# Optimization experiments

Measured on AMD Instinct MI355X. Metric: run time of the kernel, lower is better.

The kernel has to match this reference:

```python
import jax, jax.numpy as jnp
import numpy as np

# yolov5 non_max_suppression defaults (from forward's input_parameters.get defaults)
CONF_THRES = 0.25
IOU_THRES = 0.45
MAX_DET = 1000        # max detections returned per image
TOP_K = 4096          # fixed candidate count entering greedy NMS (jit-friendly stand-in for max_nms)
MAX_WH = 7680.0       # per-class box offset so NMS is class-aware (yolov5 trick)


def setup_inputs() -> dict:
    key = jax.random.key(0)
    k1, k2, k3, k4 = jax.random.split(key, 4)
    B, N, NC = 16, 25200, 80  # 640x640 yolov5 -> 25200 anchors, 80 COCO classes
    xy = jax.random.uniform(k1, (B, N, 2)) * 640.0            # box centers in pixels
    wh = jax.random.uniform(k2, (B, N, 2)) * 160.0 + 4.0       # box sizes
    obj = jax.random.uniform(k3, (B, N, 1))                    # objectness
    cls = jax.random.uniform(k4, (B, N, NC))                   # class scores
    pred = jnp.concatenate([xy, wh, obj, cls], axis=-1)        # [B, N, 85]
    return {"pred": pred}


def _xywh2xyxy(x):
    xy, wh = x[..., :2], x[..., 2:4]
    return jnp.concatenate([xy - wh * 0.5, xy + wh * 0.5], axis=-1)


def _iou_one_vs_all(box, boxes):
    # box [4], boxes [K,4], xyxy
    lt = jnp.maximum(box[:2], boxes[:, :2])
    rb = jnp.minimum(box[2:], boxes[:, 2:])
    wh = jnp.clip(rb - lt, 0.0)
    inter = wh[:, 0] * wh[:, 1]
    a1 = (box[2] - box[0]) * (box[3] - box[1])
    a2 = (boxes[:, 2] - boxes[:, 0]) * (boxes[:, 3] - boxes[:, 1])
    return inter / (a1 + a2 - inter + 1e-7)


def _nms_single(pred):
    # pred [N, 5+nc] raw yolov5 output for one image
    obj = pred[:, 4:5]
    scores_all = pred[:, 5:] * obj                 # conf = obj_conf * cls_conf
    conf = scores_all.max(axis=-1)                 # best-class confidence [N]
    cls = scores_all.argmax(axis=-1).astype(pred.dtype)
    boxes = _xywh2xyxy(pred[:, :4])                # [N,4] xyxy

    valid = conf > CONF_THRES
    s = jnp.where(valid, conf, -1.0)
    order = jnp.argsort(-s)[:TOP_K]                # top candidates by score
    b = boxes[order]                               # [K,4]
    sc = s[order]                                  # [K]
    c = cls[order]                                 # [K]
    ob = b + c[:, None] * MAX_WH                   # class-offset boxes for class-aware NMS

    ar = jnp.arange(TOP_K)

    def step(supp, i):
        alive = (~supp[i]) & (sc[i] > 0.0)
        iou = _iou_one_vs_all(ob[i], ob)
        supp = supp | (alive & (iou > IOU_THRES) & (ar > i))
        return supp, alive

    _, keep = jax.lax.scan(step, jnp.zeros(TOP_K, dtype=bool), ar)

    fs = jnp.where(keep, sc, -1.0)
    idx = jnp.argsort(-fs)[:MAX_DET]               # kept boxes, score-sorted
    det = jnp.concatenate([b[idx], fs[idx][:, None], c[idx][:, None]], axis=-1)  # [max_det,6]
    ok = fs[idx] > 0.0
    return jnp.where(ok[:, None], det, 0.0)        # zero-padded [max_det, 6] (x1,y1,x2,y2,conf,cls)


def reference(pred):
    # [B, max_det, 6] padded detections per image
    return jax.vmap(_nms_single)(pred)
```

## Files before the change

### kernel.cpp

```cpp
#include <hip/hip_runtime.h>

#define BATCH  16
#define NPRED  25200
#define NCLS   80
#define CDIM   85
#define TOPK   4096
#define NBUCK  4096
#define MAXDET 1000
#define CONF_T 0.25f
#define IOU_T  0.45f
#define MAXWH  7680.0f
#define ORD_BASE 0xBE800000u

typedef unsigned long long u64;
typedef unsigned int u32;
typedef unsigned short u16;
typedef unsigned char u8;

__device__ __forceinline__ u64 umax64(u64 a, u64 b) { return a > b ? a : b; }
__device__ __forceinline__ u64 umin64(u64 a, u64 b) { return a < b ? a : b; }

__device__ __forceinline__ void cx_u64(u64* a, int i, int p, bool desc) {
    u64 x = a[i], y = a[p];
    if (desc ? (x < y) : (x > y)) { a[i] = y; a[p] = x; }
}


__device__ void hybrid_sort4096_desc(u64 r[4], u64* a) {
    const int tid = threadIdx.x;
    for (int k = 2; k <= 4096; k <<= 1) {
        if (k >= 512) {
            int jmax = (k >> 1) > 2048 ? 2048 : (k >> 1);
#pragma unroll
            for (int e = 0; e < 4; ++e) a[4 * tid + e] = r[e];
            __syncthreads();
            for (int j = jmax; j >= 256; j >>= 1) {
#pragma unroll
                for (int t2 = 0; t2 < 2; ++t2) {
                    int q = (t2 << 10) | tid;
                    int i = ((q & ~(j - 1)) << 1) | (q & (j - 1));
                    cx_u64(a, i, i | j, (i & k) == 0);
                }
                __syncthreads();
            }
#pragma unroll
            for (int e = 0; e < 4; ++e) r[e] = a[4 * tid + e];
            __syncthreads();
        }
        {
            int jstart = (k >> 1) > 128 ? 128 : (k >> 1);
            bool desc = (((4 * tid) & k) == 0);
            for (int j = jstart; j >= 4; j >>= 1) {
                int m = j >> 2;
                bool take_max = (((tid & m) == 0) == desc);
#pragma unroll
                for (int e = 0; e < 4; ++e) {
                    u64 v = __shfl_xor(r[e], m, 64);
                    r[e] = take_max ? umax64(r[e], v) : umin64(r[e], v);
                }
            }
        }
        if (k >= 4) {
            bool desc = (((4 * tid) & k) == 0);
            u64 x0 = r[0], x2 = r[2];
            r[0] = desc ? umax64(x0, x2) : umin64(x0, x2);
            r[2] = desc ? umin64(x0, x2) : umax64(x0, x2);
            u64 x1 = r[1], x3 = r[3];
            r[1] = desc ? umax64(x1, x3) : umin64(x1, x3);
            r[3] = desc ? umin64(x1, x3) : umax64(x1, x3);
        }
        {
            bool d01 = (((4 * tid + 0) & k) == 0);
            bool d23 = (((4 * tid + 2) & k) == 0);
            u64 x0 = r[0], x1 = r[1];
            r[0] = d01 ? umax64(x0, x1) : umin64(x0, x1);
            r[1] = d01 ? umin64(x0, x1) : umax64(x0, x1);
            u64 x2 = r[2], x3 = r[3];
            r[2] = d23 ? umax64(x2, x3) : umin64(x2, x3);
            r[3] = d23 ? umin64(x2, x3) : umax64(x2, x3);
        }
    }
}

__device__ void wave_sort256_desc(u64 r[4]) {
    const int lane = threadIdx.x & 63;
    for (int k = 2; k <= 256; k <<= 1) {
        int jstart = (k >> 1) > 128 ? 128 : (k >> 1);
        bool desc = (((4 * lane) & k) == 0);
        for (int j = jstart; j >= 4; j >>= 1) {
            int m = j >> 2;
            bool take_max = (((lane & m) == 0) == desc);
#pragma unroll
            for (int e = 0; e < 4; ++e) {
                u64 v = __shfl_xor(r[e], m, 64);
                r[e] = take_max ? umax64(r[e], v) : umin64(r[e], v);
            }
        }
        if (k >= 4) {
            u64 x0 = r[0], x2 = r[2];
            r[0] = desc ? umax64(x0, x2) : umin64(x0, x2);
            r[2] = desc ? umin64(x0, x2) : umax64(x0, x2);
            u64 x1 = r[1], x3 = r[3];
            r[1] = desc ? umax64(x1, x3) : umin64(x1, x3);
            r[3] = desc ? umin64(x1, x3) : umax64(x1, x3);
        }
        {
            bool d01 = (((4 * lane + 0) & k) == 0);
            bool d23 = (((4 * lane + 2) & k) == 0);
            u64 x0 = r[0], x1 = r[1];
            r[0] = d01 ? umax64(x0, x1) : umin64(x0, x1);
            r[1] = d01 ? umin64(x0, x1) : umax64(x0, x1);
            u64 x2 = r[2], x3 = r[3];
            r[2] = d23 ? umax64(x2, x3) : umin64(x2, x3);
            r[3] = d23 ? umin64(x2, x3) : umax64(x2, x3);
        }
    }
}


__global__ __launch_bounds__(256) void k1_score(const float* __restrict__ pred,
                                                u64* __restrict__ keys,
                                                u32* __restrict__ ghist) {
    const int lane = threadIdx.x & 63;
    const int l16 = lane & 15;
    const long long gw = (long long)blockIdx.x * 4 + (threadIdx.x >> 6);
    const long long rowIdx = gw * 4 + (lane >> 4);
    const int b = (int)(rowIdx / NPRED);
    const int n = (int)(rowIdx - (long long)b * NPRED);
    const float* row = pred + rowIdx * CDIM;
    float obj = row[4];
    u64 m = 0ull;
#pragma unroll
    for (int k = 0; k < 5; ++k) {
        int c = l16 + 16 * k;
        float v = row[5 + c] * obj;
        u64 mk = ((u64)(__float_as_uint(v) | 0x80000000u) << 32) | (u64)(u32)(NCLS - 1 - c);
        if (mk > m) m = mk;
    }
#pragma unroll
    for (int o = 8; o > 0; o >>= 1) {
        u64 other = __shfl_xor(m, o, 64);
        if (other > m) m = other;
    }
    if (l16 == 0) {
        float best = __uint_as_float((u32)(m >> 32) & 0x7FFFFFFFu);
        int cls = (NCLS - 1) - (int)(m & 0x7Fu);
        float s = (best > CONF_T) ? best : -1.0f;
        u32 u = __float_as_uint(s);
        u32 ord = (u & 0x80000000u) ? ~u : (u | 0x80000000u);
        keys[rowIdx] = ((u64)ord << 32) | ((u64)(u32)(32767 - n) << 7) | (u64)(u32)cls;
        if (ord > ORD_BASE)
            atomicAdd(&ghist[b * NBUCK + ((ord - ORD_BASE - 1u) >> 12)], 1u);
    }
}


__global__ __launch_bounds__(1024) void k2cs(const u64* __restrict__ keys,
                                             const u32* __restrict__ ghist,
                                             u64* __restrict__ topSorted) {
    __shared__ u64 smem[4096];
    __shared__ u64 side[1024];
    __shared__ u32 wsum[16];
    __shared__ int sh_T, sh_C1, sh_R, c1pos, sidepos;
    const int b = blockIdx.x;
    const int tid = threadIdx.x;
    const int lane = tid & 63;
    const int wid = tid >> 6;

    u32 h[4];
    u32 tsum = 0;
#pragma unroll
    for (int e = 0; e < 4; ++e) {
        h[e] = ghist[b * NBUCK + (NBUCK - 1 - (4 * tid + e))];
        tsum += h[e];
    }
    u32 inc = tsum;
    for (int o = 1; o < 64; o <<= 1) {
        u32 v = __shfl_up(inc, o, 64);
        if (lane >= o) inc += v;
    }
    if (lane == 63) wsum[wid] = inc;
    __syncthreads();
    if (tid == 0) {
        u32 run = 0;
        for (int i = 0; i < 16; ++i) { u32 t = wsum[i]; wsum[i] = run; run += t; }
        sh_T = -1; sh_C1 = (int)run; sh_R = 0;
        c1pos = 0; sidepos = 0;
    }
    __syncthreads();
    {
        u32 cum = wsum[wid] + (inc - tsum);
#pragma unroll
        for (int e = 0; e < 4; ++e) {
            if (h[e] > 0 && cum < (u32)TOPK && cum + h[e] >= (u32)TOPK) {
                sh_T = NBUCK - 1 - (4 * tid + e);
                sh_C1 = (int)cum;
                sh_R = TOPK - (int)cum;
            }
            cum += h[e];
        }
    }
    __syncthreads();
    const int T = sh_T, C1 = sh_C1, R = sh_R;

    for (int i = tid; i < 4096; i += 1024) smem[i] = 0ull;
    side[tid] = 0ull;
    __syncthreads();
    const u64* kb = keys + (long long)b * NPRED;
    for (int n = tid; n < NPRED; n += 1024) {
        u64 key = kb[n];
        u32 hi = (u32)(key >> 32);
        if (hi > ORD_BASE) {
            int bt = (int)((hi - ORD_BASE - 1u) >> 12);
            if (bt > T) {
                int slot = atomicAdd(&c1pos, 1);
                smem[slot] = key;
            } else if (bt == T) {
                int s2 = atomicAdd(&sidepos, 1);
                if (s2 < 1024) side[s2] = key;
            }
        }
    }
    __syncthreads();

    if (R > 0) {
        int cntT = sidepos;
        if (cntT <= 256) {
            if (wid == 0) {
                u64 r[4];
#pragma unroll
                for (int e = 0; e < 4; ++e) r[e] = side[4 * lane + e];
                wave_sort256_desc(r);
#pragma unroll
                for (int e = 0; e < 4; ++e) side[4 * lane + e] = r[e];
            }
        } else {
            for (int k = 2; k <= 1024; k <<= 1) {
                for (int j = k >> 1; j >= 1; j >>= 1) {
                    if (tid < 512) {
                        int q = tid;
                        int i = ((q & ~(j - 1)) << 1) | (q & (j - 1));
                        cx_u64(side, i, i | j, (i & k) == 0);
                    }
                    __syncthreads();
                }
            }
        }
        __syncthreads();
        if (tid < R) smem[C1 + tid] = side[tid];
    }
    __syncthreads();

    u64 r[4];
#pragma unroll
    for (int e = 0; e < 4; ++e) r[e] = smem[4 * tid + e];
    hybrid_sort4096_desc(r, smem);
#pragma unroll
    for (int e = 0; e < 4; ++e) topSorted[(long long)b * TOPK + 4 * tid + e] = r[e];
}


__global__ __launch_bounds__(256) void k3a_build(const float* __restrict__ pred,
                                                 const u64* __restrict__ topSorted,
                                                 float4* __restrict__ ob,
                                                 u8* __restrict__ clsb,
                                                 u32* __restrict__ count) {
    const int idx = blockIdx.x * 256 + threadIdx.x;
    const int b = idx >> 12;
    u64 key = topSorted[idx];
    u32 hi = (u32)(key >> 32);
    u8 c = 0xFF;
    if (hi > 0x80000000u) {
        int n = 32767 - (int)((key >> 7) & 0x7FFFu);
        int ci = (int)(key & 0x7Fu);
        const float* row = pred + ((long long)b * NPRED + n) * CDIM;
        float x = row[0], y = row[1], w = row[2], h = row[3];
        float off = (float)ci * MAXWH;
        float4 o;
        o.x = (x - w * 0.5f) + off;
        o.y = (y - h * 0.5f) + off;
        o.z = (x + w * 0.5f) + off;
        o.w = (y + h * 0.5f) + off;
        ob[idx] = o;
        c = (u8)ci;
        atomicAdd(&count[b * NCLS + ci], 1u);
    }
    clsb[idx] = c;
}


__global__ __launch_bounds__(64) void k3g_gather(const u8* __restrict__ clsb,
                                                 const u32* __restrict__ count,
                                                 u32* __restrict__ startg,
                                                 u16* __restrict__ segIdx) {
    const int b = blockIdx.x;
    const int c = blockIdx.y;
    const int lane = threadIdx.x;
    u32 s = (lane < c) ? count[b * NCLS + lane] : 0u;
    if (lane + 64 < c) s += count[b * NCLS + 64 + lane];
#pragma unroll
    for (int o = 32; o > 0; o >>= 1) s += __shfl_xor(s, o, 64);
    if (lane == 0) startg[b * NCLS + c] = s;
    const u32 base = (u32)b * 4096u;
    u32 pos = s;
    const u64 lt = (1ull << lane) - 1ull;
    for (int it = 0; it < 64; ++it) {
        u8 cc = clsb[base + it * 64 + lane];
        u64 m = __ballot(cc == (u8)c);
        if (cc == (u8)c) {
            int ofs = __popcll(m & lt);
            segIdx[base + pos + ofs] = (u16)(it * 64 + lane);
        }
        pos += (u32)__popcll(m);
    }
}


__global__ __launch_bounds__(64) void k3n_nms(const float4* __restrict__ ob,
                                              const u16* __restrict__ segIdx,
                                              const u32* __restrict__ count,
                                              const u32* __restrict__ startg,
                                              u8* __restrict__ keep,
                                              u8* gsupp_) {
    const int b = blockIdx.x;
    const int c = blockIdx.y;
    const int lane = threadIdx.x;
    const int n = (int)count[b * NCLS + c];
    if (n == 0) return;
    const u32 base = startg[b * NCLS + c];
    __shared__ float4 sbox[1024];
    __shared__ u16 sidx[1024];
    __shared__ u8 ssupp_[1024];
    volatile u8* ssupp = ssupp_;
    volatile u8* gsupp = gsupp_ + b * 4096 + base;
    const float4* obb = ob + b * 4096;
    const u16* seg = segIdx + b * 4096 + base;

    for (int j = lane; j < n && j < 1024; j += 64) {
        int r = seg[j];
        sidx[j] = (u16)r;
        sbox[j] = obb[r];
        ssupp_[j] = 0;
    }
    __syncthreads();

    {
#pragma clang fp contract(off)
        for (int ii = 0; ii < n; ++ii) {
            bool sup = (ii < 1024) ? (ssupp[ii] != 0) : (gsupp[ii] != 0);
            if (sup) continue;
            int ri = (ii < 1024) ? (int)sidx[ii] : (int)seg[ii];
            if (lane == 0) keep[b * 4096 + ri] = 1;
            float4 bi = (ii < 1024) ? sbox[ii] : obb[seg[ii]];
            float a1 = (bi.z - bi.x) * (bi.w - bi.y);
            for (int jj = ii + 1 + lane; jj < n; jj += 64) {
                float4 bj = (jj < 1024) ? sbox[jj] : obb[seg[jj]];
                float ltx = fmaxf(bi.x, bj.x);
                float lty = fmaxf(bi.y, bj.y);
                float rbx = fminf(bi.z, bj.z);
                float rby = fminf(bi.w, bj.w);
                float ww = fmaxf(rbx - ltx, 0.0f);
                float hh = fmaxf(rby - lty, 0.0f);
                float inter = ww * hh;
                float a2 = (bj.z - bj.x) * (bj.w - bj.y);
                float iou = inter / (((a1 + a2) - inter) + 1e-7f);
                if (iou > IOU_T) {
                    if (jj < 1024) ssupp[jj] = 1; else gsupp[jj] = 1;
                }
            }
            __syncthreads();
        }
    }
}


__global__ __launch_bounds__(256) void k3o_out(const float* __restrict__ pred,
                                               const u64* __restrict__ topSorted,
                                               const u8* __restrict__ keep,
                                               float* __restrict__ out) {
    const int b = blockIdx.x;
    const int tid = threadIdx.x;
    __shared__ u64 words[64];
    __shared__ int wpre[64];
    float* outb = out + (long long)b * MAXDET * 6;
    for (int i = tid; i < MAXDET * 6; i += 256) outb[i] = 0.0f;
    const u8* kp = keep + b * 4096;
    if (tid < 64) {
        u64 w = 0ull;
        const u64* k8 = (const u64*)(kp + tid * 64);
#pragma unroll
        for (int q = 0; q < 8; ++q) {
            u64 v = k8[q];
#pragma unroll
            for (int bb = 0; bb < 8; ++bb)
                if ((v >> (8 * bb)) & 0xFFull) w |= 1ull << (q * 8 + bb);
        }
        words[tid] = w;
    }
    __syncthreads();
    if (tid == 0) {
        int run = 0;
        for (int t = 0; t < 64; ++t) { wpre[t] = run; run += __popcll(words[t]); }
    }
    __syncthreads();
    const u64* kb = topSorted + (long long)b * TOPK;
    for (int r = tid; r < 4096; r += 256) {
        int wd = r >> 6;
        if ((words[wd] >> (r & 63)) & 1ull) {
            int pos = wpre[wd] + __popcll(words[wd] & ((1ull << (r & 63)) - 1ull));
            if (pos < MAXDET) {
                u64 key = kb[r];
                u32 hi = (u32)(key >> 32);
                int n = 32767 - (int)((key >> 7) & 0x7FFFu);
                const float* row = pred + ((long long)b * NPRED + n) * CDIM;
                float x = row[0], y = row[1], w2 = row[2], h = row[3];
                float* o = outb + pos * 6;
                o[0] = x - w2 * 0.5f;
                o[1] = y - h * 0.5f;
                o[2] = x + w2 * 0.5f;
                o[3] = y + h * 0.5f;
                o[4] = __uint_as_float(hi & 0x7FFFFFFFu);
                o[5] = (float)(key & 0x7Fu);
            }
        }
    }
}


extern "C" void kernel_launch(void* const* d_in, const int* in_sizes, int n_in,
                              void* d_out, int out_size, void* d_ws, size_t ws_size,
                              hipStream_t stream) {
    const float* pred = (const float*)d_in[0];
    float* out = (float*)d_out;

    char* ws = (char*)d_ws;
    u64* keys      = (u64*)ws;
    u64* topSorted = (u64*)(ws + 3225600);
    float4* ob     = (float4*)(ws + 3749888);
    u8* clsb       = (u8*)(ws + 4798464);
    u16* segIdx    = (u16*)(ws + 4864000);
    u32* startg    = (u32*)(ws + 4995072);
    u32* ghist     = (u32*)(ws + 5000192);
    u32* count     = (u32*)(ws + 5262336);
    u8* keep       = (u8*)(ws + 5267456);
    u8* gsupp      = (u8*)(ws + 5332992);
    (void)hipMemsetAsync(ws + 5000192, 0, 398336, stream);

    hipLaunchKernelGGL(k1_score, dim3(BATCH * NPRED / 16), dim3(256), 0, stream,
                       pred, keys, ghist);
    hipLaunchKernelGGL(k2cs, dim3(BATCH), dim3(1024), 0, stream, keys, ghist, topSorted);
    hipLaunchKernelGGL(k3a_build, dim3(BATCH * TOPK / 256), dim3(256), 0, stream,
                       pred, topSorted, ob, clsb, count);
    hipLaunchKernelGGL(k3g_gather, dim3(BATCH, NCLS), dim3(64), 0, stream,
                       clsb, count, startg, segIdx);
    hipLaunchKernelGGL(k3n_nms, dim3(BATCH, NCLS), dim3(64), 0, stream,
                       ob, segIdx, count, startg, keep, gsupp);
    hipLaunchKernelGGL(k3o_out, dim3(BATCH), dim3(256), 0, stream, pred, topSorted, keep, out);
}
```

Measured before the change: 302.7 us.

## Fuse select, sort, class grouping, NMS and output into one per-image kernel

Folds top-k selection, bitonic sort, box building, per-class segmentation, NMS and output writing into a single 1024-thread block per image. All intermediates stay in LDS, and the global histogram atomics and memset are replaced by an LDS histogram. Classes with at most 128 boxes use a register-resident, ballot-driven wave NMS. Candidate compaction uses wave-aggregated atomics. This removes five kernel launches and their global round trips, but runs per-class NMS on only 16 blocks, 16 waves each, so there is much less parallelism than the previous 16x80 grid.

```diff
diff --git a/kernel.cpp b/kernel.cpp
--- a/kernel.cpp
+++ b/kernel.cpp
@@ -119,8 +119,7 @@
 
 
 __global__ __launch_bounds__(256) void k1_score(const float* __restrict__ pred,
-                                                u64* __restrict__ keys,
-                                                u32* __restrict__ ghist) {
+                                                u64* __restrict__ keys) {
     const int lane = threadIdx.x & 63;
     const int l16 = lane & 15;
     const long long gw = (long long)blockIdx.x * 4 + (threadIdx.x >> 6);
@@ -149,36 +148,151 @@
         u32 u = __float_as_uint(s);
         u32 ord = (u & 0x80000000u) ? ~u : (u | 0x80000000u);
         keys[rowIdx] = ((u64)ord << 32) | ((u64)(u32)(32767 - n) << 7) | (u64)(u32)cls;
-        if (ord > ORD_BASE)
-            atomicAdd(&ghist[b * NBUCK + ((ord - ORD_BASE - 1u) >> 12)], 1u);
-    }
-}
-
-
-__global__ __launch_bounds__(1024) void k2cs(const u64* __restrict__ keys,
-                                             const u32* __restrict__ ghist,
-                                             u64* __restrict__ topSorted) {
-    __shared__ u64 smem[4096];
-    __shared__ u64 side[1024];
+    }
+}
+
+
+__device__ void nms_class_wave(int n, u32 base, const u16* __restrict__ seg,
+                               const float4* __restrict__ box,
+                               u8* __restrict__ keepb, volatile u8* supp, int lane) {
+#pragma clang fp contract(off)
+    if (n <= 0) return;
+    if (n <= 128) {
+        const int j1 = 64 + lane;
+        u32 r0 = 0, r1 = 0;
+        float4 b0 = make_float4(0.0f, 0.0f, 0.0f, 0.0f);
+        float4 b1 = make_float4(0.0f, 0.0f, 0.0f, 0.0f);
+        if (lane < n) { r0 = seg[base + lane]; b0 = box[r0]; }
+        if (j1 < n)   { r1 = seg[base + j1];  b1 = box[r1]; }
+        float a20 = (b0.z - b0.x) * (b0.w - b0.y);
+        float a21 = (b1.z - b1.x) * (b1.w - b1.y);
+        u64 rem0 = (n >= 64) ? ~0ull : ((1ull << n) - 1ull);
+        u64 rem1 = (n > 64) ? ((n >= 128) ? ~0ull : ((1ull << (n - 64)) - 1ull)) : 0ull;
+        u64 keep0 = 0ull, keep1 = 0ull;
+        const bool two = (n > 64);
+        while (rem0) {
+            int ii = __builtin_ctzll(rem0);
+            rem0 &= ~(1ull << ii);
+            keep0 |= 1ull << ii;
+            float bix = __shfl(b0.x, ii, 64);
+            float biy = __shfl(b0.y, ii, 64);
+            float biz = __shfl(b0.z, ii, 64);
+            float biw = __shfl(b0.w, ii, 64);
+            float a1  = __shfl(a20, ii, 64);
+            {
+                float ltx = fmaxf(bix, b0.x), lty = fmaxf(biy, b0.y);
+                float rbx = fminf(biz, b0.z), rby = fminf(biw, b0.w);
+                float ww = fmaxf(rbx - ltx, 0.0f), hh = fmaxf(rby - lty, 0.0f);
+                float inter = ww * hh;
+                float iou = inter / (((a1 + a20) - inter) + 1e-7f);
+                bool k0 = (iou > IOU_T) && (lane > ii);
+                rem0 &= ~__ballot(k0);
+            }
+            if (two) {
+                float ltx = fmaxf(bix, b1.x), lty = fmaxf(biy, b1.y);
+                float rbx = fminf(biz, b1.z), rby = fminf(biw, b1.w);
+                float ww = fmaxf(rbx - ltx, 0.0f), hh = fmaxf(rby - lty, 0.0f);
+                float inter = ww * hh;
+                float iou = inter / (((a1 + a21) - inter) + 1e-7f);
+                bool k1 = (iou > IOU_T);
+                rem1 &= ~__ballot(k1);
+            }
+        }
+        while (rem1) {
+            int ii = __builtin_ctzll(rem1);
+            rem1 &= ~(1ull << ii);
+            keep1 |= 1ull << ii;
+            float bix = __shfl(b1.x, ii, 64);
+            float biy = __shfl(b1.y, ii, 64);
+            float biz = __shfl(b1.z, ii, 64);
+            float biw = __shfl(b1.w, ii, 64);
+            float a1  = __shfl(a21, ii, 64);
+            float ltx = fmaxf(bix, b1.x), lty = fmaxf(biy, b1.y);
+            float rbx = fminf(biz, b1.z), rby = fminf(biw, b1.w);
+            float ww = fmaxf(rbx - ltx, 0.0f), hh = fmaxf(rby - lty, 0.0f);
+            float inter = ww * hh;
+            float iou = inter / (((a1 + a21) - inter) + 1e-7f);
+            bool k1 = (iou > IOU_T) && (lane > ii);
+            rem1 &= ~__ballot(k1);
+        }
+        if ((keep0 >> lane) & 1ull) keepb[r0] = 1;
+        if ((keep1 >> lane) & 1ull) keepb[r1] = 1;
+    } else {
+        for (int ii = 0; ii < n; ++ii) {
+            if (supp[base + ii]) continue;
+            int ri = seg[base + ii];
+            if (lane == 0) keepb[ri] = 1;
+            float4 bi = box[ri];
+            float a1 = (bi.z - bi.x) * (bi.w - bi.y);
+            for (int jj = ii + 1 + lane; jj < n; jj += 64) {
+                int rj = seg[base + jj];
+                float4 bj = box[rj];
+                float ltx = fmaxf(bi.x, bj.x), lty = fmaxf(bi.y, bj.y);
+                float rbx = fminf(bi.z, bj.z), rby = fminf(bi.w, bj.w);
+                float ww = fmaxf(rbx - ltx, 0.0f), hh = fmaxf(rby - lty, 0.0f);
+                float inter = ww * hh;
+                float a2 = (bj.z - bj.x) * (bj.w - bj.y);
+                float iou = inter / (((a1 + a2) - inter) + 1e-7f);
+                if (iou > IOU_T) supp[base + jj] = 1;
+            }
+            __threadfence_block();
+        }
+    }
+}
+
+
+__global__ __launch_bounds__(1024) void k2_fused(const float* __restrict__ pred,
+                                                 const u64* __restrict__ keys,
+                                                 float* __restrict__ out) {
+    __shared__ u64 ldsbuf[15024];
     __shared__ u32 wsum[16];
     __shared__ int sh_T, sh_C1, sh_R, c1pos, sidepos;
+
+    u64*    smem   = ldsbuf;
+    float4* box    = (float4*)(ldsbuf + 4096);
+    u32*    hist   = (u32*)(ldsbuf + 4096);
+    u64*    side   = ldsbuf + 6144;
+    u16*    seg    = (u16*)(ldsbuf + 12288);
+    u8*     clsb   = (u8*)(ldsbuf + 13312);
+    u8*     suppb  = (u8*)(ldsbuf + 13824);
+    u8*     keepb  = (u8*)(ldsbuf + 14336);
+    u32*    cnt    = (u32*)(ldsbuf + 14848);
+    u32*    startc = (u32*)(ldsbuf + 14888);
+    u64*    words  = ldsbuf + 14928;
+    int*    wpre   = (int*)(ldsbuf + 14992);
+
     const int b = blockIdx.x;
     const int tid = threadIdx.x;
     const int lane = tid & 63;
     const int wid = tid >> 6;
-
-    u32 h[4];
-    u32 tsum = 0;
-#pragma unroll
-    for (int e = 0; e < 4; ++e) {
-        h[e] = ghist[b * NBUCK + (NBUCK - 1 - (4 * tid + e))];
-        tsum += h[e];
-    }
+    const u64 lanelt = (1ull << lane) - 1ull;
+    float* outb = out + (long long)b * (MAXDET * 6);
+
+    for (int i = tid; i < MAXDET * 6; i += 1024) outb[i] = 0.0f;
+
+#pragma unroll
+    for (int e = 0; e < 4; ++e) { smem[4 * tid + e] = 0ull; hist[4 * tid + e] = 0u; }
+    side[tid] = 0ull;
+    ((u32*)suppb)[tid] = 0u;
+    ((u32*)keepb)[tid] = 0u;
+    if (tid < NCLS) cnt[tid] = 0u;
+    __syncthreads();
+
+    const u64* kb = keys + (long long)b * NPRED;
+    for (int it = 0; it < (NPRED + 1023) / 1024; ++it) {
+        int n = it * 1024 + tid;
+        if (n < NPRED) {
+            u32 hi = (u32)(kb[n] >> 32);
+            if (hi > ORD_BASE) atomicAdd(&hist[(hi - ORD_BASE - 1u) >> 12], 1u);
+        }
+    }
+    __syncthreads();
+
+    u32 h[4]; u32 tsum = 0u;
+#pragma unroll
+    for (int e = 0; e < 4; ++e) { h[e] = hist[NBUCK - 1 - (4 * tid + e)]; tsum += h[e]; }
     u32 inc = tsum;
-    for (int o = 1; o < 64; o <<= 1) {
-        u32 v = __shfl_up(inc, o, 64);
-        if (lane >= o) inc += v;
-    }
+    for (int o = 1; o < 64; o <<= 1) { u32 v = __shfl_up(inc, o, 64); if (lane >= o) inc += v; }
     if (lane == 63) wsum[wid] = inc;
     __syncthreads();
     if (tid == 0) {
@@ -203,23 +317,25 @@
     __syncthreads();
     const int T = sh_T, C1 = sh_C1, R = sh_R;
 
-    for (int i = tid; i < 4096; i += 1024) smem[i] = 0ull;
-    side[tid] = 0ull;
-    __syncthreads();
-    const u64* kb = keys + (long long)b * NPRED;
-    for (int n = tid; n < NPRED; n += 1024) {
-        u64 key = kb[n];
+    for (int it = 0; it < (NPRED + 1023) / 1024; ++it) {
+        int n = it * 1024 + tid;
+        bool act = n < NPRED;
+        u64 key = act ? kb[n] : 0ull;
         u32 hi = (u32)(key >> 32);
-        if (hi > ORD_BASE) {
-            int bt = (int)((hi - ORD_BASE - 1u) >> 12);
-            if (bt > T) {
-                int slot = atomicAdd(&c1pos, 1);
-                smem[slot] = key;
-            } else if (bt == T) {
-                int s2 = atomicAdd(&sidepos, 1);
-                if (s2 < 1024) side[s2] = key;
-            }
-        }
+        bool v = act && (hi > ORD_BASE);
+        int bt = v ? (int)((hi - ORD_BASE - 1u) >> 12) : -1;
+        bool t1 = v && (bt > T);
+        bool t2 = v && (bt == T);
+        u64 m1 = __ballot(t1), m2 = __ballot(t2);
+        int b1 = 0, b2 = 0;
+        if (lane == 0) {
+            if (m1) b1 = atomicAdd(&c1pos, (int)__popcll(m1));
+            if (m2) b2 = atomicAdd(&sidepos, (int)__popcll(m2));
+        }
+        b1 = __shfl(b1, 0, 64);
+        b2 = __shfl(b2, 0, 64);
+        if (t1) smem[b1 + __popcll(m1 & lanelt)] = key;
+        if (t2) { int s2 = b2 + __popcll(m2 & lanelt); if (s2 < 1024) side[s2] = key; }
     }
     __syncthreads();
 
@@ -251,143 +367,70 @@
     }
     __syncthreads();
 
-    u64 r[4];
-#pragma unroll
-    for (int e = 0; e < 4; ++e) r[e] = smem[4 * tid + e];
-    hybrid_sort4096_desc(r, smem);
-#pragma unroll
-    for (int e = 0; e < 4; ++e) topSorted[(long long)b * TOPK + 4 * tid + e] = r[e];
-}
-
-
-__global__ __launch_bounds__(256) void k3a_build(const float* __restrict__ pred,
-                                                 const u64* __restrict__ topSorted,
-                                                 float4* __restrict__ ob,
-                                                 u8* __restrict__ clsb,
-                                                 u32* __restrict__ count) {
-    const int idx = blockIdx.x * 256 + threadIdx.x;
-    const int b = idx >> 12;
-    u64 key = topSorted[idx];
-    u32 hi = (u32)(key >> 32);
-    u8 c = 0xFF;
-    if (hi > 0x80000000u) {
-        int n = 32767 - (int)((key >> 7) & 0x7FFFu);
-        int ci = (int)(key & 0x7Fu);
-        const float* row = pred + ((long long)b * NPRED + n) * CDIM;
-        float x = row[0], y = row[1], w = row[2], h = row[3];
-        float off = (float)ci * MAXWH;
-        float4 o;
-        o.x = (x - w * 0.5f) + off;
-        o.y = (y - h * 0.5f) + off;
-        o.z = (x + w * 0.5f) + off;
-        o.w = (y + h * 0.5f) + off;
-        ob[idx] = o;
-        c = (u8)ci;
-        atomicAdd(&count[b * NCLS + ci], 1u);
-    }
-    clsb[idx] = c;
-}
-
-
-__global__ __launch_bounds__(64) void k3g_gather(const u8* __restrict__ clsb,
-                                                 const u32* __restrict__ count,
-                                                 u32* __restrict__ startg,
-                                                 u16* __restrict__ segIdx) {
-    const int b = blockIdx.x;
-    const int c = blockIdx.y;
-    const int lane = threadIdx.x;
-    u32 s = (lane < c) ? count[b * NCLS + lane] : 0u;
-    if (lane + 64 < c) s += count[b * NCLS + 64 + lane];
-#pragma unroll
-    for (int o = 32; o > 0; o >>= 1) s += __shfl_xor(s, o, 64);
-    if (lane == 0) startg[b * NCLS + c] = s;
-    const u32 base = (u32)b * 4096u;
-    u32 pos = s;
-    const u64 lt = (1ull << lane) - 1ull;
-    for (int it = 0; it < 64; ++it) {
-        u8 cc = clsb[base + it * 64 + lane];
-        u64 m = __ballot(cc == (u8)c);
-        if (cc == (u8)c) {
-            int ofs = __popcll(m & lt);
-            segIdx[base + pos + ofs] = (u16)(it * 64 + lane);
-        }
-        pos += (u32)__popcll(m);
-    }
-}
-
-
-__global__ __launch_bounds__(64) void k3n_nms(const float4* __restrict__ ob,
-                                              const u16* __restrict__ segIdx,
-                                              const u32* __restrict__ count,
-                                              const u32* __restrict__ startg,
-                                              u8* __restrict__ keep,
-                                              u8* gsupp_) {
-    const int b = blockIdx.x;
-    const int c = blockIdx.y;
-    const int lane = threadIdx.x;
-    const int n = (int)count[b * NCLS + c];
-    if (n == 0) return;
-    const u32 base = startg[b * NCLS + c];
-    __shared__ float4 sbox[1024];
-    __shared__ u16 sidx[1024];
-    __shared__ u8 ssupp_[1024];
-    volatile u8* ssupp = ssupp_;
-    volatile u8* gsupp = gsupp_ + b * 4096 + base;
-    const float4* obb = ob + b * 4096;
-    const u16* seg = segIdx + b * 4096 + base;
-
-    for (int j = lane; j < n && j < 1024; j += 64) {
-        int r = seg[j];
-        sidx[j] = (u16)r;
-        sbox[j] = obb[r];
-        ssupp_[j] = 0;
-    }
-    __syncthreads();
-
     {
-#pragma clang fp contract(off)
-        for (int ii = 0; ii < n; ++ii) {
-            bool sup = (ii < 1024) ? (ssupp[ii] != 0) : (gsupp[ii] != 0);
-            if (sup) continue;
-            int ri = (ii < 1024) ? (int)sidx[ii] : (int)seg[ii];
-            if (lane == 0) keep[b * 4096 + ri] = 1;
-            float4 bi = (ii < 1024) ? sbox[ii] : obb[seg[ii]];
-            float a1 = (bi.z - bi.x) * (bi.w - bi.y);
-            for (int jj = ii + 1 + lane; jj < n; jj += 64) {
-                float4 bj = (jj < 1024) ? sbox[jj] : obb[seg[jj]];
-                float ltx = fmaxf(bi.x, bj.x);
-                float lty = fmaxf(bi.y, bj.y);
-                float rbx = fminf(bi.z, bj.z);
-                float rby = fminf(bi.w, bj.w);
-                float ww = fmaxf(rbx - ltx, 0.0f);
-                float hh = fmaxf(rby - lty, 0.0f);
-                float inter = ww * hh;
-                float a2 = (bj.z - bj.x) * (bj.w - bj.y);
-                float iou = inter / (((a1 + a2) - inter) + 1e-7f);
-                if (iou > IOU_T) {
-                    if (jj < 1024) ssupp[jj] = 1; else gsupp[jj] = 1;
-                }
-            }
-            __syncthreads();
-        }
-    }
-}
-
-
-__global__ __launch_bounds__(256) void k3o_out(const float* __restrict__ pred,
-                                               const u64* __restrict__ topSorted,
-                                               const u8* __restrict__ keep,
-                                               float* __restrict__ out) {
-    const int b = blockIdx.x;
-    const int tid = threadIdx.x;
-    __shared__ u64 words[64];
-    __shared__ int wpre[64];
-    float* outb = out + (long long)b * MAXDET * 6;
-    for (int i = tid; i < MAXDET * 6; i += 256) outb[i] = 0.0f;
-    const u8* kp = keep + b * 4096;
+        u64 r[4];
+#pragma unroll
+        for (int e = 0; e < 4; ++e) r[e] = smem[4 * tid + e];
+        hybrid_sort4096_desc(r, smem);
+#pragma unroll
+        for (int e = 0; e < 4; ++e) smem[4 * tid + e] = r[e];
+    }
+    __syncthreads();
+
+#pragma unroll
+    for (int e = 0; e < 4; ++e) {
+        int idx = e * 1024 + tid;
+        u64 key = smem[idx];
+        u32 hi = (u32)(key >> 32);
+        u8 c = 0xFF;
+        if (hi > 0x80000000u) {
+            int n = 32767 - (int)((key >> 7) & 0x7FFFu);
+            int ci = (int)(key & 0x7Fu);
+            const float* row = pred + ((long long)b * NPRED + n) * CDIM;
+            float x = row[0], y = row[1], w = row[2], hh = row[3];
+            float off = (float)ci * MAXWH;
+            float4 o;
+            o.x = (x - w * 0.5f) + off;
+            o.y = (y - hh * 0.5f) + off;
+            o.z = (x + w * 0.5f) + off;
+            o.w = (y + hh * 0.5f) + off;
+            box[idx] = o;
+            c = (u8)ci;
+            atomicAdd(&cnt[ci], 1u);
+        }
+        clsb[idx] = c;
+    }
+    __syncthreads();
+
+    if (tid == 0) {
+        u32 run = 0;
+        for (int c = 0; c < NCLS; ++c) { startc[c] = run; run += cnt[c]; }
+    }
+    __syncthreads();
+
+    {
+        u32 pos0 = startc[wid +  0], pos1 = startc[wid + 16], pos2 = startc[wid + 32],
+            pos3 = startc[wid + 48], pos4 = startc[wid + 64];
+        for (int itr = 0; itr < 64; ++itr) {
+            int j = itr * 64 + lane;
+            int cc = (int)clsb[j];
+            u64 m;
+            m = __ballot(cc == wid +  0); if (cc == wid +  0) seg[pos0 + __popcll(m & lanelt)] = (u16)j; pos0 += (u32)__popcll(m);
+            m = __ballot(cc == wid + 16); if (cc == wid + 16) seg[pos1 + __popcll(m & lanelt)] = (u16)j; pos1 += (u32)__popcll(m);
+            m = __ballot(cc == wid + 32); if (cc == wid + 32) seg[pos2 + __popcll(m & lanelt)] = (u16)j; pos2 += (u32)__popcll(m);
+            m = __ballot(cc == wid + 48); if (cc == wid + 48) seg[pos3 + __popcll(m & lanelt)] = (u16)j; pos3 += (u32)__popcll(m);
+            m = __ballot(cc == wid + 64); if (cc == wid + 64) seg[pos4 + __popcll(m & lanelt)] = (u16)j; pos4 += (u32)__popcll(m);
+        }
+        for (int q = 0; q < 5; ++q) {
+            int c = wid + 16 * q;
+            nms_class_wave((int)cnt[c], startc[c], seg, box, keepb, (volatile u8*)suppb, lane);
+        }
+    }
+    __syncthreads();
+
     if (tid < 64) {
         u64 w = 0ull;
-        const u64* k8 = (const u64*)(kp + tid * 64);
+        const u64* k8 = (const u64*)(keepb + tid * 64);
 #pragma unroll
         for (int q = 0; q < 8; ++q) {
             u64 v = k8[q];
@@ -403,22 +446,22 @@
         for (int t = 0; t < 64; ++t) { wpre[t] = run; run += __popcll(words[t]); }
     }
     __syncthreads();
-    const u64* kb = topSorted + (long long)b * TOPK;
-    for (int r = tid; r < 4096; r += 256) {
-        int wd = r >> 6;
-        if ((words[wd] >> (r & 63)) & 1ull) {
-            int pos = wpre[wd] + __popcll(words[wd] & ((1ull << (r & 63)) - 1ull));
+    for (int rr = tid; rr < TOPK; rr += 1024) {
+        int wd = rr >> 6;
+        u64 wv = words[wd];
+        if ((wv >> (rr & 63)) & 1ull) {
+            int pos = wpre[wd] + __popcll(wv & ((1ull << (rr & 63)) - 1ull));
             if (pos < MAXDET) {
-                u64 key = kb[r];
+                u64 key = smem[rr];
                 u32 hi = (u32)(key >> 32);
                 int n = 32767 - (int)((key >> 7) & 0x7FFFu);
                 const float* row = pred + ((long long)b * NPRED + n) * CDIM;
-                float x = row[0], y = row[1], w2 = row[2], h = row[3];
+                float x = row[0], y = row[1], w2 = row[2], hh = row[3];
                 float* o = outb + pos * 6;
                 o[0] = x - w2 * 0.5f;
-                o[1] = y - h * 0.5f;
+                o[1] = y - hh * 0.5f;
                 o[2] = x + w2 * 0.5f;
-                o[3] = y + h * 0.5f;
+                o[3] = y + hh * 0.5f;
                 o[4] = __uint_as_float(hi & 0x7FFFFFFFu);
                 o[5] = (float)(key & 0x7Fu);
             }
@@ -433,27 +476,9 @@
     const float* pred = (const float*)d_in[0];
     float* out = (float*)d_out;
 
-    char* ws = (char*)d_ws;
-    u64* keys      = (u64*)ws;
-    u64* topSorted = (u64*)(ws + 3225600);
-    float4* ob     = (float4*)(ws + 3749888);
-    u8* clsb       = (u8*)(ws + 4798464);
-    u16* segIdx    = (u16*)(ws + 4864000);
-    u32* startg    = (u32*)(ws + 4995072);
-    u32* ghist     = (u32*)(ws + 5000192);
-    u32* count     = (u32*)(ws + 5262336);
-    u8* keep       = (u8*)(ws + 5267456);
-    u8* gsupp      = (u8*)(ws + 5332992);
-    (void)hipMemsetAsync(ws + 5000192, 0, 398336, stream);
+    u64* keys = (u64*)d_ws;
 
     hipLaunchKernelGGL(k1_score, dim3(BATCH * NPRED / 16), dim3(256), 0, stream,
-                       pred, keys, ghist);
-    hipLaunchKernelGGL(k2cs, dim3(BATCH), dim3(1024), 0, stream, keys, ghist, topSorted);
-    hipLaunchKernelGGL(k3a_build, dim3(BATCH * TOPK / 256), dim3(256), 0, stream,
-                       pred, topSorted, ob, clsb, count);
-    hipLaunchKernelGGL(k3g_gather, dim3(BATCH, NCLS), dim3(64), 0, stream,
-                       clsb, count, startg, segIdx);
-    hipLaunchKernelGGL(k3n_nms, dim3(BATCH, NCLS), dim3(64), 0, stream,
-                       ob, segIdx, count, startg, keep, gsupp);
-    hipLaunchKernelGGL(k3o_out, dim3(BATCH), dim3(256), 0, stream, pred, topSorted, keep, out);
-}
+                       pred, keys);
+    hipLaunchKernelGGL(k2_fused, dim3(BATCH), dim3(1024), 0, stream, pred, keys, out);
+}
```

Measured after the change: 351.8 us. 16.2% more time.
